# Performance work log

Measured on AMD Instinct MI355X. Metric: run time of the kernel, lower is better.

## Reference

```python
import jax, jax.numpy as jnp
import numpy as np

B, S, K, N, GROUP = 4, 8, 4096, 11008, 128
NUM_GROUPS = K // GROUP  # 32


def setup_inputs() -> dict:
    key = jax.random.key(0)
    k1, k2, k3 = jax.random.split(key, 3)
    x = jax.random.normal(k1, (B, S, K), dtype=jnp.float16)
    # packed int4 weights: each byte holds two nibbles (low nibble = even k, high = odd k)
    weight_packed = jax.random.randint(k2, (N, K // 2), 0, 256, dtype=jnp.int32)
    # scales: abs(randn)*0.1 in fp16, as in the torch module
    scales = (jnp.abs(jax.random.normal(k3, (N, NUM_GROUPS), dtype=jnp.float16)) * jnp.float16(0.1))
    return {"x": x, "weight_packed": weight_packed, "scales": scales}


def _dequant(weight_packed, scales, Kd):
    # unpack: low nibble -> even index k, high nibble -> odd index k+1
    n = weight_packed.shape[0]
    low = weight_packed & 0xF
    high = (weight_packed >> 4) & 0xF
    w = jnp.stack([low, high], axis=-1).reshape(n, Kd)  # [N, K] int in [0,16)
    g = Kd // scales.shape[1]
    # group-wise dequant: scale * (w - 8), scale applied in fp32 (matches fp32-accum kernel)
    wq = (w.astype(jnp.float32) - 8.0).reshape(n, scales.shape[1], g)
    wdeq = wq * scales.astype(jnp.float32)[:, :, None]
    return wdeq.reshape(n, Kd)  # [N, K] fp32


def reference(x, weight_packed, scales):
    b, s, kd = x.shape
    wdeq = _dequant(weight_packed, scales, kd)           # [N, K]
    x2 = x.reshape(-1, kd).astype(jnp.float32)           # [M, K], fp32 accumulation
    out = jnp.einsum('mk,nk->mn', x2, wdeq)              # [M, N]
    return out.astype(jnp.float16).reshape(b, s, -1)
```

## Files before the change

### kernel.cpp

```cpp
#include <hip/hip_runtime.h>

#define M 32
#define N 11008
#define K 4096
#define NGROUPS 32
#define BN 16
#define KSPLIT 2
#define KRANGE (K / KSPLIT)
#define KWAVE (KRANGE / 4)
#define DEPTH 4
#define WSLOT 256
#define XSLOT 512
#define LWAVE (DEPTH * (WSLOT + XSLOT))
#define RS 17

typedef _Float16 half8 __attribute__((ext_vector_type(8)));
typedef _Float16 half4 __attribute__((ext_vector_type(4)));
typedef float floatx4 __attribute__((ext_vector_type(4)));

__device__ inline void gll16(const void* g, void* l) {
    __builtin_amdgcn_global_load_lds(
        (const __attribute__((address_space(1))) unsigned int*)g,
        (__attribute__((address_space(3))) unsigned int*)l, 16, 0, 0);
}

__device__ inline half8 unpack8(int4 wv) {
    uint4 uw; unsigned int b;
    b = (unsigned)wv.x; uw.x = ((b | (b << 12)) & 0x000F000Fu) | 0x64006400u;
    b = (unsigned)wv.y; uw.y = ((b | (b << 12)) & 0x000F000Fu) | 0x64006400u;
    b = (unsigned)wv.z; uw.z = ((b | (b << 12)) & 0x000F000Fu) | 0x64006400u;
    b = (unsigned)wv.w; uw.w = ((b | (b << 12)) & 0x000F000Fu) | 0x64006400u;
    const half8 c1032 = (half8)(_Float16)1032.0f;
    return __builtin_bit_cast(half8, uw) - c1032;
}

__global__ __launch_bounds__(512) void xcvt_kernel(
    const float* __restrict__ x, _Float16* __restrict__ xf)
{
    int i = (blockIdx.x * 512 + threadIdx.x) * 4;
    float4 v = *(const float4*)(x + i);
    half4 h;
    h[0] = (_Float16)v.x; h[1] = (_Float16)v.y;
    h[2] = (_Float16)v.z; h[3] = (_Float16)v.w;
    *(half4*)(xf + i) = h;
}


#define WAITV(n) asm volatile("s_waitcnt vmcnt(" #n ")" ::: "memory")
#define SB() __builtin_amdgcn_sched_barrier(0)

#define ISSUE(s) {                                                  \
    gll16(gw  + (s) * 16, wbase + ((s) & 3) * WSLOT);               \
    gll16(gx0 + (s) * 32, xbase + ((s) & 3) * XSLOT);               \
    gll16(gx1 + (s) * 32, xbase + ((s) & 3) * XSLOT + 256);         \
}

#define COMPUTE(s) {                                                \
    int4 wv  = *(const int4*)&wbase[((s) & 3) * WSLOT + lane4];     \
    half8 a0 = *(const half8*)&xh[((s) & 3) * 1024 + lane8];        \
    half8 a1 = *(const half8*)&xh[((s) & 3) * 1024 + 512 + lane8];  \
    SB();                                                           \
    half8 b = unpack8(wv);                                          \
    t0 = __builtin_amdgcn_mfma_f32_16x16x32_f16(a0, b, t0, 0, 0, 0);\
    t1 = __builtin_amdgcn_mfma_f32_16x16x32_f16(a1, b, t1, 0, 0, 0);\
}

#define APPLY(sg) {                                                 \
    _Pragma("unroll")                                               \
    for (int r = 0; r < 4; ++r) {                                   \
        acc0[r] += (sg) * t0[r];                                    \
        acc1[r] += (sg) * t1[r];                                    \
    }                                                               \
    t0 = (floatx4){0.f,0.f,0.f,0.f};                                \
    t1 = (floatx4){0.f,0.f,0.f,0.f};                                \
}

__global__ __launch_bounds__(256) void int4_gemm_kernel(
    const _Float16* __restrict__ xf,
    const int* __restrict__ wp,
    const float* __restrict__ scales,
    float* __restrict__ out)
{
    __shared__ int lds[4 * LWAVE];

    const int t    = threadIdx.x;
    const int lane = t & 63;
    const int w    = t >> 6;
    const int n0   = blockIdx.x * BN;
    const int ks   = blockIdx.y;
    const int row  = lane & 15;
    const int quad = lane >> 4;
    const int lane4 = lane * 4;
    const int lane8 = lane * 8;

    const int kw = ks * KRANGE + w * KWAVE;

    int* wbase = &lds[w * LWAVE];
    int* xbase = wbase + DEPTH * WSLOT;
    const _Float16* xh = (const _Float16*)xbase;

    const int*      gw  = wp + (long)(n0 + row) * (K / 2) + (kw >> 1) + quad * 4;
    const _Float16* gx0 = xf + (long)row * K + kw + quad * 8;
    const _Float16* gx1 = gx0 + 16 * K;

    const float* sp = scales + (long)(n0 + row) * NGROUPS + (kw >> 7);
    const float sg0 = sp[0], sg1 = sp[1], sg2 = sp[2], sg3 = sp[3];

    floatx4 acc0 = {0,0,0,0}, acc1 = {0,0,0,0};
    floatx4 t0   = {0,0,0,0}, t1   = {0,0,0,0};

    ISSUE(0) ISSUE(1) ISSUE(2) ISSUE(3)

    WAITV(9); COMPUTE(0)              SB(); ISSUE(4)
    WAITV(9); COMPUTE(1)              SB(); ISSUE(5)
    WAITV(9); COMPUTE(2)              SB(); ISSUE(6)
    WAITV(9); COMPUTE(3)  APPLY(sg0) SB(); ISSUE(7)
    WAITV(9); COMPUTE(4)              SB(); ISSUE(8)
    WAITV(9); COMPUTE(5)              SB(); ISSUE(9)
    WAITV(9); COMPUTE(6)              SB(); ISSUE(10)
    WAITV(9); COMPUTE(7)  APPLY(sg1) SB(); ISSUE(11)
    WAITV(9); COMPUTE(8)              SB(); ISSUE(12)
    WAITV(9); COMPUTE(9)              SB(); ISSUE(13)
    WAITV(9); COMPUTE(10)             SB(); ISSUE(14)
    WAITV(9); COMPUTE(11) APPLY(sg2) SB(); ISSUE(15)
    WAITV(9); COMPUTE(12)
    WAITV(6); COMPUTE(13)
    WAITV(3); COMPUTE(14)
    WAITV(0); COMPUTE(15) APPLY(sg3)

    __syncthreads();
    float* red = (float*)lds;
    float* rw  = red + w * 32 * RS;
    #pragma unroll
    for (int r = 0; r < 4; ++r) {
        rw[(quad * 4 + r) * RS + row]      = acc0[r];
        rw[(quad * 4 + r + 16) * RS + row] = acc1[r];
    }
    __syncthreads();
    #pragma unroll
    for (int i = 0; i < 2; ++i) {
        const int o = t + 256 * i;
        const int m = o >> 4;
        const int n = o & 15;
        const int a = m * RS + n;
        const float sum = red[a] + red[32 * RS + a] + red[64 * RS + a] + red[96 * RS + a];
        atomicAdd(&out[(long)m * N + n0 + n], sum);
    }
}

extern "C" void kernel_launch(void* const* d_in, const int* in_sizes, int n_in,
                              void* d_out, int out_size, void* d_ws, size_t ws_size,
                              hipStream_t stream) {
    const float* x      = (const float*)d_in[0];
    const int* wp       = (const int*)d_in[1];
    const float* scales = (const float*)d_in[2];
    float* out          = (float*)d_out;
    _Float16* xf16      = (_Float16*)d_ws;

    (void)hipMemsetAsync(out, 0, (size_t)M * N * sizeof(float), stream);
    xcvt_kernel<<<dim3((M * K) / (512 * 4)), 512, 0, stream>>>(x, xf16);
    int4_gemm_kernel<<<dim3(N / BN, KSPLIT), 256, 0, stream>>>(xf16, wp, scales, out);
}
```

Baseline: 160.7 us.

## Split K eight ways and stage weight tiles cooperatively in LDS with direct x loads

Raises the K-split from 2 to 8, so each block covers 512 K values, and replaces the per-wave 4-deep LDS ring with a block-cooperative two-tile weight load into padded LDS. Activations are read straight from global memory into registers instead of through LDS. The aim is more blocks in flight for better latency hiding and occupancy (launch bounds hint 8 blocks per CU). In exchange, four times as many atomicAdds hit the output, and there is less per-block pipelining.

```diff
diff --git a/kernel.cpp b/kernel.cpp
--- a/kernel.cpp
+++ b/kernel.cpp
@@ -5,13 +5,10 @@
 #define K 4096
 #define NGROUPS 32
 #define BN 16
-#define KSPLIT 2
+#define KSPLIT 8
 #define KRANGE (K / KSPLIT)
-#define KWAVE (KRANGE / 4)
-#define DEPTH 4
-#define WSLOT 256
-#define XSLOT 512
-#define LWAVE (DEPTH * (WSLOT + XSLOT))
+#define WPAIR 260
+#define WTILE (8 * WPAIR)
 #define RS 17
 
 typedef _Float16 half8 __attribute__((ext_vector_type(8)));
@@ -45,43 +42,15 @@
     *(half4*)(xf + i) = h;
 }
 
+#define WAITV(n) asm volatile("s_waitcnt vmcnt(" #n ")" ::: "memory")
 
-#define WAITV(n) asm volatile("s_waitcnt vmcnt(" #n ")" ::: "memory")
-#define SB() __builtin_amdgcn_sched_barrier(0)
-
-#define ISSUE(s) {                                                  \
-    gll16(gw  + (s) * 16, wbase + ((s) & 3) * WSLOT);               \
-    gll16(gx0 + (s) * 32, xbase + ((s) & 3) * XSLOT);               \
-    gll16(gx1 + (s) * 32, xbase + ((s) & 3) * XSLOT + 256);         \
-}
-
-#define COMPUTE(s) {                                                \
-    int4 wv  = *(const int4*)&wbase[((s) & 3) * WSLOT + lane4];     \
-    half8 a0 = *(const half8*)&xh[((s) & 3) * 1024 + lane8];        \
-    half8 a1 = *(const half8*)&xh[((s) & 3) * 1024 + 512 + lane8];  \
-    SB();                                                           \
-    half8 b = unpack8(wv);                                          \
-    t0 = __builtin_amdgcn_mfma_f32_16x16x32_f16(a0, b, t0, 0, 0, 0);\
-    t1 = __builtin_amdgcn_mfma_f32_16x16x32_f16(a1, b, t1, 0, 0, 0);\
-}
-
-#define APPLY(sg) {                                                 \
-    _Pragma("unroll")                                               \
-    for (int r = 0; r < 4; ++r) {                                   \
-        acc0[r] += (sg) * t0[r];                                    \
-        acc1[r] += (sg) * t1[r];                                    \
-    }                                                               \
-    t0 = (floatx4){0.f,0.f,0.f,0.f};                                \
-    t1 = (floatx4){0.f,0.f,0.f,0.f};                                \
-}
-
-__global__ __launch_bounds__(256) void int4_gemm_kernel(
+__global__ __launch_bounds__(256, 8) void int4_gemm_kernel(
     const _Float16* __restrict__ xf,
     const int* __restrict__ wp,
     const float* __restrict__ scales,
     float* __restrict__ out)
 {
-    __shared__ int lds[4 * LWAVE];
+    __shared__ int wsh[2 * WTILE];
 
     const int t    = threadIdx.x;
     const int lane = t & 63;
@@ -90,46 +59,77 @@
     const int ks   = blockIdx.y;
     const int row  = lane & 15;
     const int quad = lane >> 4;
-    const int lane4 = lane * 4;
-    const int lane8 = lane * 8;
+    const int kb   = ks * KRANGE;
 
-    const int kw = ks * KRANGE + w * KWAVE;
+    const int p0 = w * 2, p1 = p0 + 1;
+    const int h32 = lane >> 5;
+    const int* ga = wp + (long)(n0 + 2 * p0 + h32) * (K / 2) + (kb >> 1) + (lane & 31) * 4;
+    const int* gb = wp + (long)(n0 + 2 * p1 + h32) * (K / 2) + (kb >> 1) + (lane & 31) * 4;
+    gll16(ga,       &wsh[p0 * WPAIR]);
+    gll16(gb,       &wsh[p1 * WPAIR]);
+    gll16(ga + 128, &wsh[WTILE + p0 * WPAIR]);
+    gll16(gb + 128, &wsh[WTILE + p1 * WPAIR]);
 
-    int* wbase = &lds[w * LWAVE];
-    int* xbase = wbase + DEPTH * WSLOT;
-    const _Float16* xh = (const _Float16*)xbase;
+    const float* sp = scales + (long)(n0 + row) * NGROUPS + ks * 4 + (w >> 1);
+    const float sc0 = sp[0];
+    const float sc1 = sp[2];
 
-    const int*      gw  = wp + (long)(n0 + row) * (K / 2) + (kw >> 1) + quad * 4;
-    const _Float16* gx0 = xf + (long)row * K + kw + quad * 8;
+    const _Float16* gx0 = xf + (long)row * K + kb + w * 64 + quad * 8;
     const _Float16* gx1 = gx0 + 16 * K;
-
-    const float* sp = scales + (long)(n0 + row) * NGROUPS + (kw >> 7);
-    const float sg0 = sp[0], sg1 = sp[1], sg2 = sp[2], sg3 = sp[3];
+    half8 a00 = *(const half8*)(gx0);
+    half8 a01 = *(const half8*)(gx0 + 32);
+    half8 a10 = *(const half8*)(gx1);
+    half8 a11 = *(const half8*)(gx1 + 32);
 
     floatx4 acc0 = {0,0,0,0}, acc1 = {0,0,0,0};
-    floatx4 t0   = {0,0,0,0}, t1   = {0,0,0,0};
 
-    ISSUE(0) ISSUE(1) ISSUE(2) ISSUE(3)
+    WAITV(2);
+    __builtin_amdgcn_s_barrier();
+    __builtin_amdgcn_sched_barrier(0);
 
-    WAITV(9); COMPUTE(0)              SB(); ISSUE(4)
-    WAITV(9); COMPUTE(1)              SB(); ISSUE(5)
-    WAITV(9); COMPUTE(2)              SB(); ISSUE(6)
-    WAITV(9); COMPUTE(3)  APPLY(sg0) SB(); ISSUE(7)
-    WAITV(9); COMPUTE(4)              SB(); ISSUE(8)
-    WAITV(9); COMPUTE(5)              SB(); ISSUE(9)
-    WAITV(9); COMPUTE(6)              SB(); ISSUE(10)
-    WAITV(9); COMPUTE(7)  APPLY(sg1) SB(); ISSUE(11)
-    WAITV(9); COMPUTE(8)              SB(); ISSUE(12)
-    WAITV(9); COMPUTE(9)              SB(); ISSUE(13)
-    WAITV(9); COMPUTE(10)             SB(); ISSUE(14)
-    WAITV(9); COMPUTE(11) APPLY(sg2) SB(); ISSUE(15)
-    WAITV(9); COMPUTE(12)
-    WAITV(6); COMPUTE(13)
-    WAITV(3); COMPUTE(14)
-    WAITV(0); COMPUTE(15) APPLY(sg3)
+    {
+        floatx4 t0 = {0,0,0,0}, t1 = {0,0,0,0};
+        #pragma unroll
+        for (int kk = 0; kk < 2; ++kk) {
+            const int bidx = (row >> 1) * WPAIR + (row & 1) * 128 + w * 32 + kk * 16 + quad * 4;
+            half8 b = unpack8(*(const int4*)&wsh[bidx]);
+            t0 = __builtin_amdgcn_mfma_f32_16x16x32_f16(kk ? a01 : a00, b, t0, 0, 0, 0);
+            t1 = __builtin_amdgcn_mfma_f32_16x16x32_f16(kk ? a11 : a10, b, t1, 0, 0, 0);
+        }
+        #pragma unroll
+        for (int r = 0; r < 4; ++r) {
+            acc0[r] += sc0 * t0[r];
+            acc1[r] += sc0 * t1[r];
+        }
+    }
+
+    half8 c00 = *(const half8*)(gx0 + 256);
+    half8 c01 = *(const half8*)(gx0 + 256 + 32);
+    half8 c10 = *(const half8*)(gx1 + 256);
+    half8 c11 = *(const half8*)(gx1 + 256 + 32);
+
+    WAITV(4);
+    __builtin_amdgcn_s_barrier();
+    __builtin_amdgcn_sched_barrier(0);
+
+    {
+        floatx4 t0 = {0,0,0,0}, t1 = {0,0,0,0};
+        #pragma unroll
+        for (int kk = 0; kk < 2; ++kk) {
+            const int bidx = WTILE + (row >> 1) * WPAIR + (row & 1) * 128 + w * 32 + kk * 16 + quad * 4;
+            half8 b = unpack8(*(const int4*)&wsh[bidx]);
+            t0 = __builtin_amdgcn_mfma_f32_16x16x32_f16(kk ? c01 : c00, b, t0, 0, 0, 0);
+            t1 = __builtin_amdgcn_mfma_f32_16x16x32_f16(kk ? c11 : c10, b, t1, 0, 0, 0);
+        }
+        #pragma unroll
+        for (int r = 0; r < 4; ++r) {
+            acc0[r] += sc1 * t0[r];
+            acc1[r] += sc1 * t1[r];
+        }
+    }
 
     __syncthreads();
-    float* red = (float*)lds;
+    float* red = (float*)wsh;
     float* rw  = red + w * 32 * RS;
     #pragma unroll
     for (int r = 0; r < 4; ++r) {
```

Result: faster. 146.8 us (-8.6%).
